# Performance work log

Hardware: AMD Instinct MI355X
Metric: run time of the kernel (lower is better)

## Reference

```python
import jax, jax.numpy as jnp
import numpy as np

N, D = 32768, 256  # n_nodes, in_dim == mem_dim


def setup_inputs() -> dict:
    key = jax.random.key(0)
    ks = jax.random.split(key, 8)
    inputs = jax.random.normal(ks[0], (N, D), jnp.float32)
    state = jax.random.normal(ks[1], (1, D), jnp.float32)  # initial root cell state
    s = 1.0 / np.sqrt(D)  # pytorch default uniform init bound
    root_W = jax.random.uniform(ks[2], (D, D), jnp.float32, -s, s)
    root_b = jax.random.uniform(ks[3], (D,), jnp.float32, -s, s)
    W_ih = jax.random.uniform(ks[4], (4 * D, D), jnp.float32, -s, s)
    W_hh = jax.random.uniform(ks[5], (4 * D, D), jnp.float32, -s, s)
    b_ih = jax.random.uniform(ks[6], (4 * D,), jnp.float32, -s, s)
    b_hh = jax.random.uniform(ks[7], (4 * D,), jnp.float32, -s, s)
    # topologically ordered random tree: parents[i] < i, node 0 is root
    rng = np.random.default_rng(0)
    raw = rng.integers(0, N, size=N)
    parents = jnp.asarray(np.minimum(raw, np.maximum(np.arange(N) - 1, 0)).astype(np.int64))
    idx = jnp.arange(N, dtype=jnp.int64)  # node -> input row (tree.idx)
    return dict(inputs=inputs, state=state, root_W=root_W, root_b=root_b,
                W_ih=W_ih, W_hh=W_hh, b_ih=b_ih, b_hh=b_hh,
                parents=parents, idx=idx)


def reference(inputs, state, root_W, root_b, W_ih, W_hh, b_ih, b_hh, parents, idx):
    n, d = inputs.shape
    # root: tanh(Linear(inputs[root_idx])), cell state = given state
    h0 = jnp.tanh(inputs[idx[0]] @ root_W.T + root_b)
    c0 = state[0]
    H = jnp.zeros((n, d), inputs.dtype).at[0].set(h0)
    C = jnp.zeros((n, d), inputs.dtype).at[0].set(c0)

    def step(carry, i):
        H, C = carry
        p = parents[i]
        x = inputs[idx[i]]
        # torch nn.LSTMCell: gates = x W_ih^T + b_ih + h W_hh^T + b_hh
        gates = x @ W_ih.T + b_ih + H[p] @ W_hh.T + b_hh
        ig, fg, gg, og = jnp.split(gates, 4)
        c = jax.nn.sigmoid(fg) * C[p] + jax.nn.sigmoid(ig) * jnp.tanh(gg)
        h = jax.nn.sigmoid(og) * jnp.tanh(c)
        return (H.at[i].set(h), C.at[i].set(c)), None

    (H, C), _ = jax.lax.scan(step, (H, C), jnp.arange(1, n))
    # topdown_hidden_traversal: scatter each node's hidden into a [n_inputs, mem_dim] buffer
    hiddens = jnp.zeros((n, d), inputs.dtype).at[idx].set(H)
    # (root topdown_state, root topdown hidden, all hiddens)
    return C[0:1], H[0:1], hiddens
```

## Files before the change

### kernel.cpp

```cpp
#include <hip/hip_runtime.h>


#define NN 32768
#define DD 256
#define GP 1024
#define OFFCAP 4096
#define SENT_C 0x7FC00001u
#define SENT_H 0xFFFFFFFFu

typedef __attribute__((ext_vector_type(8))) short short8;
typedef __attribute__((ext_vector_type(4))) float float4_;
typedef __attribute__((ext_vector_type(4))) unsigned uint4_;

static __device__ __forceinline__ unsigned short f2bf(float f) {
    unsigned u = __builtin_bit_cast(unsigned, f);
    unsigned r = u + 0x7FFFu + ((u >> 16) & 1u);
    return (unsigned short)(r >> 16);
}
static __device__ __forceinline__ float bf2f(unsigned short u) {
    unsigned v = ((unsigned)u) << 16;
    return __builtin_bit_cast(float, v);
}
static __device__ __forceinline__ float sigf(float x) { return 1.0f / (1.0f + __expf(-x)); }
static __device__ __forceinline__ float tanh_(float x) { return 1.0f - 2.0f / (__expf(2.0f * x) + 1.0f); }

__global__ void k_init(int* cnt, int* cur, int* maxd, float* C, unsigned* HbU) {
    const int g = blockIdx.x * 256 + threadIdx.x;
    if (g < NN + 2) { cnt[g] = 0; cur[g] = 0; }
    if (g == 0) maxd[0] = 0;
    const uint4_ sc = (uint4_){SENT_C, SENT_C, SENT_C, SENT_C};
    const uint4_ sh = (uint4_){SENT_H, SENT_H, SENT_H, SENT_H};
    uint4_* Cu = (uint4_*)C;
    uint4_* Hu = (uint4_*)HbU;
    #pragma unroll
    for (int k = 0; k < 4; ++k) Cu[(size_t)g + (size_t)k * 524288] = sc;
    #pragma unroll
    for (int k = 0; k < 2; ++k) Hu[(size_t)g + (size_t)k * 524288] = sh;
}

__global__ void k_root(const float* __restrict__ X, const float* __restrict__ state,
                       const float* __restrict__ rootW, const float* __restrict__ rootb,
                       const int* __restrict__ idx,
                       unsigned short* __restrict__ Hb, float* __restrict__ C) {
    const int t = threadIdx.x;
    const int row = idx[0];
    const float4_* xr = (const float4_*)(X + (size_t)row * DD);
    const float4_* wr = (const float4_*)(rootW + (size_t)t * DD);
    float acc = rootb[t];
    for (int k = 0; k < DD / 4; ++k) {
        float4_ a = xr[k], b = wr[k];
        acc += a[0] * b[0] + a[1] * b[1] + a[2] * b[2] + a[3] * b[3];
    }
    Hb[t] = f2bf(tanh_(acc));
    C[t] = state[t];
}

__global__ void k_dep_init(const int* __restrict__ parents, int* dep, int* jmp) {
    int i = blockIdx.x * 256 + threadIdx.x;
    if (i >= NN) return;
    dep[i] = (i == 0) ? 0 : 1;
    jmp[i] = (i == 0) ? 0 : parents[i];
}

__global__ void k_dep_step(const int* __restrict__ depA, const int* __restrict__ jmpA,
                           int* __restrict__ depB, int* __restrict__ jmpB) {
    int i = blockIdx.x * 256 + threadIdx.x;
    if (i >= NN) return;
    int j = jmpA[i];
    depB[i] = depA[i] + depA[j];
    jmpB[i] = jmpA[j];
}

__global__ void k_hist(const int* __restrict__ dep, int* cnt, int* maxd) {
    int i = blockIdx.x * 256 + threadIdx.x;
    if (i >= NN) return;
    int d = dep[i];
    atomicAdd(&cnt[d], 1);
    atomicMax(&maxd[0], d);
}

__global__ void k_scan(const int* __restrict__ cnt, int* __restrict__ off) {
    __shared__ int sums[256];
    const int tid = threadIdx.x;
    const int base = tid * 128;
    int s = 0;
    for (int k = 0; k < 128; ++k) s += cnt[base + k];
    sums[tid] = s;
    __syncthreads();
    if (tid == 0) {
        int run = 0;
        for (int t = 0; t < 256; ++t) { int tmp = sums[t]; sums[t] = run; run += tmp; }
    }
    __syncthreads();
    int run = sums[tid];
    for (int k = 0; k < 128; ++k) { off[base + k] = run; run += cnt[base + k]; }
    if (tid == 255) off[NN] = run;
}

__global__ void k_scatter(const int* __restrict__ dep, const int* __restrict__ off,
                          int* cur, int* __restrict__ lev) {
    int i = blockIdx.x * 256 + threadIdx.x;
    if (i >= NN) return;
    int d = dep[i];
    int pos = off[d] + atomicAdd(&cur[d], 1);
    lev[pos] = i;
}

__global__ __launch_bounds__(256, 1) void k_gx(
    const float* __restrict__ X, const float* __restrict__ Wih,
    const float* __restrict__ bih, const float* __restrict__ bhh,
    const int* __restrict__ idx, unsigned short* __restrict__ Gp) {
    __shared__ __align__(16) short bw_s[128 * 264];
    __shared__ float bias_s[128];
    const int tid = threadIdx.x;
    const int w = tid >> 6, l = tid & 63;
    const int lanelo = l & 15, quad = l >> 4;

    short8 a[2][8];
    #pragma unroll
    for (int ti = 0; ti < 2; ++ti) {
        int n = (blockIdx.x * 8 + w * 2 + ti) * 16 + lanelo;
        int row = idx[n];
        const float* xp = X + (size_t)row * DD + quad * 8;
        #pragma unroll
        for (int ks = 0; ks < 8; ++ks) {
            float4_ x0 = *(const float4_*)(xp + ks * 32);
            float4_ x1 = *(const float4_*)(xp + ks * 32 + 4);
            short8 s;
            s[0] = f2bf(x0[0]); s[1] = f2bf(x0[1]); s[2] = f2bf(x0[2]); s[3] = f2bf(x0[3]);
            s[4] = f2bf(x1[0]); s[5] = f2bf(x1[1]); s[6] = f2bf(x1[2]); s[7] = f2bf(x1[3]);
            a[ti][ks] = s;
        }
    }
    for (int gc = 0; gc < 8; ++gc) {
        __syncthreads();
        for (int e = tid; e < 128 * 64; e += 256) {
            int r = e >> 6, c4 = (e & 63) * 4;
            float4_ b = *(const float4_*)(Wih + (size_t)(gc * 128 + r) * DD + c4);
            unsigned short* pb = (unsigned short*)&bw_s[r * 264 + c4];
            pb[0] = f2bf(b[0]); pb[1] = f2bf(b[1]); pb[2] = f2bf(b[2]); pb[3] = f2bf(b[3]);
        }
        if (tid < 128) bias_s[tid] = bih[gc * 128 + tid] + bhh[gc * 128 + tid];
        __syncthreads();
        #pragma unroll
        for (int ntl = 0; ntl < 8; ++ntl) {
            float4_ acc0 = (float4_){0.f, 0.f, 0.f, 0.f};
            float4_ acc1 = (float4_){0.f, 0.f, 0.f, 0.f};
            #pragma unroll
            for (int ks = 0; ks < 8; ++ks) {
                short8 bf = *(const short8*)&bw_s[(ntl * 16 + lanelo) * 264 + ks * 32 + quad * 8];
                acc0 = __builtin_amdgcn_mfma_f32_16x16x32_bf16(a[0][ks], bf, acc0, 0, 0, 0);
                acc1 = __builtin_amdgcn_mfma_f32_16x16x32_bf16(a[1][ks], bf, acc1, 0, 0, 0);
            }
            float bia = bias_s[ntl * 16 + lanelo];
            int g = gc * 128 + ntl * 16 + lanelo;
            int nb0 = (blockIdx.x * 8 + w * 2) * 16 + quad * 4;
            #pragma unroll
            for (int r = 0; r < 4; ++r) {
                Gp[(size_t)(nb0 + r) * GP + g] = f2bf(acc0[r] + bia);
                Gp[(size_t)(nb0 + 16 + r) * GP + g] = f2bf(acc1[r] + bia);
            }
        }
    }
}

__global__ __launch_bounds__(256, 1) void k_tree2(
    const float* __restrict__ Whh,
    const int* __restrict__ parents,
    const int* __restrict__ off, const int* __restrict__ lev, const int* __restrict__ maxd_g,
    const unsigned short* __restrict__ Gp,
    unsigned short* __restrict__ Hb, float* __restrict__ C) {

    __shared__ __align__(16) short w_s[128 * 264];
    __shared__ __align__(16) short A_s[16 * 264];
    __shared__ __align__(16) float G_s[16 * 128];
    __shared__ __align__(16) float R_s[16 * 132];
    __shared__ int off_s[OFFCAP];
    __shared__ int nd_s[16], par_s[16];

    const int tid = threadIdx.x;
    const int j = blockIdx.x & 7, grp = blockIdx.x >> 3;
    const int w = tid >> 6, l = tid & 63;
    const int lanelo = l & 15, quad = l >> 4;

    for (int e = tid; e < 128 * 64; e += 256) {
        int r = e >> 6, c4 = (e & 63) * 4;
        int G = ((r >> 5) * 256) + j * 32 + (r & 31);
        float4_ b = *(const float4_*)(Whh + (size_t)G * DD + c4);
        unsigned short* pb = (unsigned short*)&w_s[r * 264 + c4];
        pb[0] = f2bf(b[0]); pb[1] = f2bf(b[1]); pb[2] = f2bf(b[2]); pb[3] = f2bf(b[3]);
    }
    const int maxd = maxd_g[0];
    const int staged = (maxd + 2 < OFFCAP) ? (maxd + 2) : OFFCAP;
    for (int e = tid; e < staged; e += 256) off_s[e] = off[e];
    __syncthreads();

    #define OFFS(i) (((i) < staged) ? off_s[(i)] : off[(i)])

    const unsigned* HbU = (const unsigned*)Hb;
    int pn_node = -1, pn_par = 0;
    bool pn_valid = false;

    int lo = OFFS(1);
    for (int d = 1; d <= maxd; ++d) {
        const int hi = OFFS(d + 1);
        const int tiles = (hi - lo + 15) >> 4;
        for (int t = grp; t < tiles; t += 32) {
            const int base = lo + t * 16;
            if (tid < 16) {
                if (pn_valid) {
                    nd_s[tid] = pn_node; par_s[tid] = pn_par;
                } else {
                    int node = -1, p = 0;
                    if (base + tid < hi) { node = lev[base + tid]; p = parents[node]; }
                    nd_s[tid] = node; par_s[tid] = p;
                }
            }
            pn_valid = false;
            __syncthreads();
            {
                int m = tid >> 4, q8 = (tid & 15) * 8;
                int seg = q8 >> 5, cc = q8 & 31;
                float4_ g01 = (float4_){0.f, 0.f, 0.f, 0.f};
                float4_ g23 = (float4_){0.f, 0.f, 0.f, 0.f};
                if (nd_s[m] >= 0) {
                    const unsigned short* gp =
                        Gp + (size_t)nd_s[m] * GP + seg * 256 + j * 32 + cc;
                    short8 gv = *(const short8*)gp;
                    g01[0] = bf2f(gv[0]); g01[1] = bf2f(gv[1]); g01[2] = bf2f(gv[2]); g01[3] = bf2f(gv[3]);
                    g23[0] = bf2f(gv[4]); g23[1] = bf2f(gv[5]); g23[2] = bf2f(gv[6]); g23[3] = bf2f(gv[7]);
                }
                *(float4_*)&G_s[m * 128 + q8] = g01;
                *(float4_*)&G_s[m * 128 + q8 + 4] = g23;
            }
            {
                int nt_base = -1, nt_hi = hi;
                if (t + 32 < tiles) {
                    nt_base = lo + (t + 32) * 16;
                } else if (d < maxd) {
                    const int hi2 = OFFS(d + 2);
                    const int tiles2 = (hi2 - hi + 15) >> 4;
                    if (grp < tiles2) { nt_base = hi + grp * 16; nt_hi = hi2; }
                }
                if (nt_base >= 0) {
                    if (tid < 16) {
                        int node = -1, p = 0;
                        if (nt_base + tid < nt_hi) { node = lev[nt_base + tid]; p = parents[node]; }
                        pn_node = node; pn_par = p;
                    }
                    pn_valid = true;
                }
            }
            const int m0 = tid >> 5, c0 = tid & 31, col = j * 32 + c0;
            float* cpp0 = &C[(size_t)par_s[m0] * DD + col];
            float* cpp1 = &C[(size_t)par_s[m0 + 8] * DD + col];
            float cp0 = __hip_atomic_load(cpp0, __ATOMIC_RELAXED, __HIP_MEMORY_SCOPE_AGENT);
            float cp1 = __hip_atomic_load(cpp1, __ATOMIC_RELAXED, __HIP_MEMORY_SCOPE_AGENT);
            unsigned hv[8];
            bool ok = true;
            #pragma unroll
            for (int k2 = 0; k2 < 8; ++k2) {
                const int e = tid + k2 * 256, m = e >> 7, cu = e & 127;
                hv[k2] = (nd_s[m] >= 0)
                    ? __hip_atomic_load(&HbU[(size_t)par_s[m] * 128 + cu],
                                        __ATOMIC_RELAXED, __HIP_MEMORY_SCOPE_AGENT)
                    : 0u;
                if (nd_s[m] >= 0 && hv[k2] == SENT_H) ok = false;
            }
            if (nd_s[m0] >= 0 && __builtin_bit_cast(unsigned, cp0) == SENT_C) ok = false;
            if (nd_s[m0 + 8] >= 0 && __builtin_bit_cast(unsigned, cp1) == SENT_C) ok = false;
            if (!__syncthreads_and(ok ? 1 : 0)) {
                if (tid < 64) {
                    const int m = tid & 15;
                    const bool act = (tid < 16) && (nd_s[m] >= 0);
                    const unsigned* sp = &HbU[(size_t)par_s[m] * 128 + j * 16];
                    bool miss = act && (__hip_atomic_load(sp, __ATOMIC_RELAXED,
                                                          __HIP_MEMORY_SCOPE_AGENT) == SENT_H);
                    while (__any(miss ? 1 : 0))
                        miss = act && (__hip_atomic_load(sp, __ATOMIC_RELAXED,
                                                         __HIP_MEMORY_SCOPE_AGENT) == SENT_H);
                }
                __syncthreads();
                if (nd_s[m0] >= 0)
                    while (__builtin_bit_cast(unsigned, cp0) == SENT_C) {
                        __builtin_amdgcn_s_sleep(1);
                        cp0 = __hip_atomic_load(cpp0, __ATOMIC_RELAXED, __HIP_MEMORY_SCOPE_AGENT);
                    }
                if (nd_s[m0 + 8] >= 0)
                    while (__builtin_bit_cast(unsigned, cp1) == SENT_C) {
                        __builtin_amdgcn_s_sleep(1);
                        cp1 = __hip_atomic_load(cpp1, __ATOMIC_RELAXED, __HIP_MEMORY_SCOPE_AGENT);
                    }
                #pragma unroll
                for (int k2 = 0; k2 < 8; ++k2) {
                    const int e = tid + k2 * 256, m = e >> 7, cu = e & 127;
                    if (nd_s[m] >= 0)
                        while (hv[k2] == SENT_H) {
                            __builtin_amdgcn_s_sleep(1);
                            hv[k2] = __hip_atomic_load(&HbU[(size_t)par_s[m] * 128 + cu],
                                                       __ATOMIC_RELAXED, __HIP_MEMORY_SCOPE_AGENT);
                        }
                }
            }
            #pragma unroll
            for (int k2 = 0; k2 < 8; ++k2) {
                const int e = tid + k2 * 256, m = e >> 7, cu = e & 127;
                *(unsigned*)&A_s[m * 264 + cu * 2] = hv[k2];
            }
            __syncthreads();
            {
                short8 af[8];
                #pragma unroll
                for (int ks = 0; ks < 8; ++ks)
                    af[ks] = *(const short8*)&A_s[lanelo * 264 + ks * 32 + quad * 8];
                #pragma unroll
                for (int ti = 0; ti < 2; ++ti) {
                    int ntl = w * 2 + ti;
                    float4_ acc = (float4_){0.f, 0.f, 0.f, 0.f};
                    #pragma unroll
                    for (int ks = 0; ks < 8; ++ks) {
                        short8 bf = *(const short8*)&w_s[(ntl * 16 + lanelo) * 264 + ks * 32 + quad * 8];
                        acc = __builtin_amdgcn_mfma_f32_16x16x32_bf16(af[ks], bf, acc, 0, 0, 0);
                    }
                    #pragma unroll
                    for (int r = 0; r < 4; ++r)
                        R_s[(quad * 4 + r) * 132 + ntl * 16 + lanelo] = acc[r];
                }
            }
            __syncthreads();
            {
                #pragma unroll
                for (int pass = 0; pass < 2; ++pass) {
                    int m = m0 + pass * 8;
                    float cp = pass ? cp1 : cp0;
                    float ig = R_s[m * 132 + c0]      + G_s[m * 128 + c0];
                    float fg = R_s[m * 132 + 32 + c0] + G_s[m * 128 + 32 + c0];
                    float gg = R_s[m * 132 + 64 + c0] + G_s[m * 128 + 64 + c0];
                    float og = R_s[m * 132 + 96 + c0] + G_s[m * 128 + 96 + c0];
                    float cn = sigf(fg) * cp + sigf(ig) * tanh_(gg);
                    float hn = sigf(og) * tanh_(cn);
                    int node = nd_s[m];
                    unsigned short hs = f2bf(hn);
                    unsigned pair = ((unsigned)hs) |
                                    (((unsigned)(unsigned short)__shfl_down((int)hs, 1)) << 16);
                    if (node >= 0) {
                        __hip_atomic_store(&C[(size_t)node * DD + col], cn,
                                           __ATOMIC_RELAXED, __HIP_MEMORY_SCOPE_AGENT);
                        if ((c0 & 1) == 0)
                            __hip_atomic_store(&((unsigned*)Hb)[(size_t)node * 128 + (col >> 1)],
                                               pair, __ATOMIC_RELAXED, __HIP_MEMORY_SCOPE_AGENT);
                    }
                }
            }
            __builtin_amdgcn_fence(__ATOMIC_RELEASE, "workgroup");
            __syncthreads();
        }
        lo = hi;
    }
    #undef OFFS
}

__global__ void k_out(const unsigned short* __restrict__ Hb, const float* __restrict__ C,
                      const int* __restrict__ idx, float* __restrict__ out) {
    const int b = blockIdx.x, t = threadIdx.x;
    if (b < NN) {
        int drow = idx[b];
        out[512 + (size_t)drow * DD + t] = bf2f(Hb[(size_t)b * DD + t]);
    } else {
        out[t] = C[t];
        out[DD + t] = bf2f(Hb[t]);
    }
}

extern "C" void kernel_launch(void* const* d_in, const int* in_sizes, int n_in,
                              void* d_out, int out_size, void* d_ws, size_t ws_size,
                              hipStream_t stream) {
    const float* X     = (const float*)d_in[0];
    const float* state = (const float*)d_in[1];
    const float* rootW = (const float*)d_in[2];
    const float* rootb = (const float*)d_in[3];
    const float* Wih   = (const float*)d_in[4];
    const float* Whh   = (const float*)d_in[5];
    const float* bih   = (const float*)d_in[6];
    const float* bhh   = (const float*)d_in[7];
    const int* parents = (const int*)d_in[8];
    const int* idx     = (const int*)d_in[9];

    float* C           = (float*)d_ws;
    unsigned short* Hb = (unsigned short*)(C + (size_t)NN * DD);
    unsigned short* Gp = Hb + (size_t)NN * DD;
    int* ip            = (int*)(Gp + (size_t)NN * GP);
    int* depA = ip;            ip += NN;
    int* jmpA = ip;            ip += NN;
    int* depB = ip;            ip += NN;
    int* jmpB = ip;            ip += NN;
    int* cnt  = ip;            ip += NN + 2;
    int* off  = ip;            ip += NN + 2;
    int* cur  = ip;            ip += NN + 2;
    int* lev  = ip;            ip += NN;
    int* maxd = ip;            ip += 4;
    float* out = (float*)d_out;

    k_init<<<dim3(2048), dim3(256), 0, stream>>>(cnt, cur, maxd, C, (unsigned*)Hb);
    k_root<<<dim3(1), dim3(256), 0, stream>>>(X, state, rootW, rootb, idx, Hb, C);

    k_dep_init<<<dim3(128), dim3(256), 0, stream>>>(parents, depA, jmpA);
    int* dA = depA; int* jA = jmpA; int* dB = depB; int* jB = jmpB;
    for (int it = 0; it < 15; ++it) {
        k_dep_step<<<dim3(128), dim3(256), 0, stream>>>(dA, jA, dB, jB);
        int* tp;
        tp = dA; dA = dB; dB = tp;
        tp = jA; jA = jB; jB = tp;
    }
    k_hist<<<dim3(128), dim3(256), 0, stream>>>(dA, cnt, maxd);
    k_scan<<<dim3(1), dim3(256), 0, stream>>>(cnt, off);
    k_scatter<<<dim3(128), dim3(256), 0, stream>>>(dA, off, cur, lev);

    k_gx<<<dim3(256), dim3(256), 0, stream>>>(X, Wih, bih, bhh, idx, Gp);
    k_tree2<<<dim3(256), dim3(256), 0, stream>>>(Whh, parents, off, lev, maxd, Gp, Hb, C);
    k_out<<<dim3(NN + 1), dim3(256), 0, stream>>>(Hb, C, idx, out);
}
```

Baseline: 1.764 ms.

## Fuse LSTM gate epilogue into MFMA registers by permuting W_hh rows

Reorders the W_hh rows staged in shared memory so each wave's two MFMA accumulators hold matching i/g and f/o gate columns. The gate nonlinearities are then computed directly from registers using lane shuffles, which removes the R_s shared-memory round trip and one __syncthreads per tile. Parent cell-state loads now follow the MFMA output layout, so only half the lanes do them. The init kernel is also split, and the sentinel poisoning plus root kernel are moved to run right before the tree kernel.

```diff
diff --git a/kernel.cpp b/kernel.cpp
--- a/kernel.cpp
+++ b/kernel.cpp
@@ -12,6 +12,9 @@
 typedef __attribute__((ext_vector_type(4))) float float4_;
 typedef __attribute__((ext_vector_type(4))) unsigned uint4_;
 
+#define ATL(p) __hip_atomic_load((p), __ATOMIC_RELAXED, __HIP_MEMORY_SCOPE_AGENT)
+#define ATS(p, v) __hip_atomic_store((p), (v), __ATOMIC_RELAXED, __HIP_MEMORY_SCOPE_AGENT)
+
 static __device__ __forceinline__ unsigned short f2bf(float f) {
     unsigned u = __builtin_bit_cast(unsigned, f);
     unsigned r = u + 0x7FFFu + ((u >> 16) & 1u);
@@ -24,10 +27,14 @@
 static __device__ __forceinline__ float sigf(float x) { return 1.0f / (1.0f + __expf(-x)); }
 static __device__ __forceinline__ float tanh_(float x) { return 1.0f - 2.0f / (__expf(2.0f * x) + 1.0f); }
 
-__global__ void k_init(int* cnt, int* cur, int* maxd, float* C, unsigned* HbU) {
-    const int g = blockIdx.x * 256 + threadIdx.x;
+__global__ void k_init_sched(int* cnt, int* cur, int* maxd) {
+    int g = blockIdx.x * 256 + threadIdx.x;
     if (g < NN + 2) { cnt[g] = 0; cur[g] = 0; }
     if (g == 0) maxd[0] = 0;
+}
+
+__global__ void k_poison(float* C, unsigned* HbU) {
+    const int g = blockIdx.x * 256 + threadIdx.x;
     const uint4_ sc = (uint4_){SENT_C, SENT_C, SENT_C, SENT_C};
     const uint4_ sh = (uint4_){SENT_H, SENT_H, SENT_H, SENT_H};
     uint4_* Cu = (uint4_*)C;
@@ -174,7 +181,6 @@
     __shared__ __align__(16) short w_s[128 * 264];
     __shared__ __align__(16) short A_s[16 * 264];
     __shared__ __align__(16) float G_s[16 * 128];
-    __shared__ __align__(16) float R_s[16 * 132];
     __shared__ int off_s[OFFCAP];
     __shared__ int nd_s[16], par_s[16];
 
@@ -182,10 +188,16 @@
     const int j = blockIdx.x & 7, grp = blockIdx.x >> 3;
     const int w = tid >> 6, l = tid & 63;
     const int lanelo = l & 15, quad = l >> 4;
+    const bool ewl = (lanelo < 8);
+    const int colw = j * 32 + w * 8 + (lanelo & 7);
+    const int gcw = w * 8 + (lanelo & 7);
+    const int gof0 = (lanelo >> 3) * 32 + gcw;
+    const int gof1 = gof0 + 64;
 
     for (int e = tid; e < 128 * 64; e += 256) {
         int r = e >> 6, c4 = (e & 63) * 4;
-        int G = ((r >> 5) * 256) + j * 32 + (r & 31);
+        int wp = r >> 5, ti = (r >> 4) & 1, n = r & 15;
+        int G = (ti * 2 + (n >> 3)) * 256 + j * 32 + wp * 8 + (n & 7);
         float4_ b = *(const float4_*)(Whh + (size_t)G * DD + c4);
         unsigned short* pb = (unsigned short*)&w_s[r * 264 + c4];
         pb[0] = f2bf(b[0]); pb[1] = f2bf(b[1]); pb[2] = f2bf(b[2]); pb[3] = f2bf(b[3]);
@@ -198,6 +210,8 @@
     #define OFFS(i) (((i) < staged) ? off_s[(i)] : off[(i)])
 
     const unsigned* HbU = (const unsigned*)Hb;
+    unsigned* HbW = (unsigned*)Hb;
+    const unsigned* Cw = (const unsigned*)C;
     int pn_node = -1, pn_par = 0;
     bool pn_valid = false;
 
@@ -251,54 +265,49 @@
                     pn_valid = true;
                 }
             }
-            const int m0 = tid >> 5, c0 = tid & 31, col = j * 32 + c0;
-            float* cpp0 = &C[(size_t)par_s[m0] * DD + col];
-            float* cpp1 = &C[(size_t)par_s[m0 + 8] * DD + col];
-            float cp0 = __hip_atomic_load(cpp0, __ATOMIC_RELAXED, __HIP_MEMORY_SCOPE_AGENT);
-            float cp1 = __hip_atomic_load(cpp1, __ATOMIC_RELAXED, __HIP_MEMORY_SCOPE_AGENT);
             unsigned hv[8];
             bool ok = true;
             #pragma unroll
             for (int k2 = 0; k2 < 8; ++k2) {
                 const int e = tid + k2 * 256, m = e >> 7, cu = e & 127;
                 hv[k2] = (nd_s[m] >= 0)
-                    ? __hip_atomic_load(&HbU[(size_t)par_s[m] * 128 + cu],
-                                        __ATOMIC_RELAXED, __HIP_MEMORY_SCOPE_AGENT)
-                    : 0u;
+                    ? ATL(&HbU[(size_t)par_s[m] * 128 + cu]) : 0u;
                 if (nd_s[m] >= 0 && hv[k2] == SENT_H) ok = false;
             }
-            if (nd_s[m0] >= 0 && __builtin_bit_cast(unsigned, cp0) == SENT_C) ok = false;
-            if (nd_s[m0 + 8] >= 0 && __builtin_bit_cast(unsigned, cp1) == SENT_C) ok = false;
+            unsigned cwv[4];
+            #pragma unroll
+            for (int r = 0; r < 4; ++r) {
+                const int m = quad * 4 + r;
+                cwv[r] = (ewl && nd_s[m] >= 0)
+                    ? ATL(&Cw[(size_t)par_s[m] * DD + colw]) : 0u;
+                if (ewl && nd_s[m] >= 0 && cwv[r] == SENT_C) ok = false;
+            }
             if (!__syncthreads_and(ok ? 1 : 0)) {
                 if (tid < 64) {
                     const int m = tid & 15;
                     const bool act = (tid < 16) && (nd_s[m] >= 0);
                     const unsigned* sp = &HbU[(size_t)par_s[m] * 128 + j * 16];
-                    bool miss = act && (__hip_atomic_load(sp, __ATOMIC_RELAXED,
-                                                          __HIP_MEMORY_SCOPE_AGENT) == SENT_H);
+                    bool miss = act && (ATL(sp) == SENT_H);
                     while (__any(miss ? 1 : 0))
-                        miss = act && (__hip_atomic_load(sp, __ATOMIC_RELAXED,
-                                                         __HIP_MEMORY_SCOPE_AGENT) == SENT_H);
+                        miss = act && (ATL(sp) == SENT_H);
                 }
                 __syncthreads();
-                if (nd_s[m0] >= 0)
-                    while (__builtin_bit_cast(unsigned, cp0) == SENT_C) {
-                        __builtin_amdgcn_s_sleep(1);
-                        cp0 = __hip_atomic_load(cpp0, __ATOMIC_RELAXED, __HIP_MEMORY_SCOPE_AGENT);
-                    }
-                if (nd_s[m0 + 8] >= 0)
-                    while (__builtin_bit_cast(unsigned, cp1) == SENT_C) {
-                        __builtin_amdgcn_s_sleep(1);
-                        cp1 = __hip_atomic_load(cpp1, __ATOMIC_RELAXED, __HIP_MEMORY_SCOPE_AGENT);
-                    }
                 #pragma unroll
                 for (int k2 = 0; k2 < 8; ++k2) {
                     const int e = tid + k2 * 256, m = e >> 7, cu = e & 127;
                     if (nd_s[m] >= 0)
                         while (hv[k2] == SENT_H) {
                             __builtin_amdgcn_s_sleep(1);
-                            hv[k2] = __hip_atomic_load(&HbU[(size_t)par_s[m] * 128 + cu],
-                                                       __ATOMIC_RELAXED, __HIP_MEMORY_SCOPE_AGENT);
+                            hv[k2] = ATL(&HbU[(size_t)par_s[m] * 128 + cu]);
+                        }
+                }
+                #pragma unroll
+                for (int r = 0; r < 4; ++r) {
+                    const int m = quad * 4 + r;
+                    if (ewl && nd_s[m] >= 0)
+                        while (cwv[r] == SENT_C) {
+                            __builtin_amdgcn_s_sleep(1);
+                            cwv[r] = ATL(&Cw[(size_t)par_s[m] * DD + colw]);
                         }
                 }
             }
@@ -308,48 +317,38 @@
                 *(unsigned*)&A_s[m * 264 + cu * 2] = hv[k2];
             }
             __syncthreads();
+            float4_ acc0 = (float4_){0.f, 0.f, 0.f, 0.f};
+            float4_ acc1 = (float4_){0.f, 0.f, 0.f, 0.f};
             {
                 short8 af[8];
                 #pragma unroll
                 for (int ks = 0; ks < 8; ++ks)
                     af[ks] = *(const short8*)&A_s[lanelo * 264 + ks * 32 + quad * 8];
                 #pragma unroll
-                for (int ti = 0; ti < 2; ++ti) {
-                    int ntl = w * 2 + ti;
-                    float4_ acc = (float4_){0.f, 0.f, 0.f, 0.f};
-                    #pragma unroll
-                    for (int ks = 0; ks < 8; ++ks) {
-                        short8 bf = *(const short8*)&w_s[(ntl * 16 + lanelo) * 264 + ks * 32 + quad * 8];
-                        acc = __builtin_amdgcn_mfma_f32_16x16x32_bf16(af[ks], bf, acc, 0, 0, 0);
-                    }
-                    #pragma unroll
-                    for (int r = 0; r < 4; ++r)
-                        R_s[(quad * 4 + r) * 132 + ntl * 16 + lanelo] = acc[r];
-                }
-            }
-            __syncthreads();
-            {
-                #pragma unroll
-                for (int pass = 0; pass < 2; ++pass) {
-                    int m = m0 + pass * 8;
-                    float cp = pass ? cp1 : cp0;
-                    float ig = R_s[m * 132 + c0]      + G_s[m * 128 + c0];
-                    float fg = R_s[m * 132 + 32 + c0] + G_s[m * 128 + 32 + c0];
-                    float gg = R_s[m * 132 + 64 + c0] + G_s[m * 128 + 64 + c0];
-                    float og = R_s[m * 132 + 96 + c0] + G_s[m * 128 + 96 + c0];
-                    float cn = sigf(fg) * cp + sigf(ig) * tanh_(gg);
-                    float hn = sigf(og) * tanh_(cn);
-                    int node = nd_s[m];
-                    unsigned short hs = f2bf(hn);
-                    unsigned pair = ((unsigned)hs) |
-                                    (((unsigned)(unsigned short)__shfl_down((int)hs, 1)) << 16);
-                    if (node >= 0) {
-                        __hip_atomic_store(&C[(size_t)node * DD + col], cn,
-                                           __ATOMIC_RELAXED, __HIP_MEMORY_SCOPE_AGENT);
-                        if ((c0 & 1) == 0)
-                            __hip_atomic_store(&((unsigned*)Hb)[(size_t)node * 128 + (col >> 1)],
-                                               pair, __ATOMIC_RELAXED, __HIP_MEMORY_SCOPE_AGENT);
-                    }
+                for (int ks = 0; ks < 8; ++ks) {
+                    short8 b0 = *(const short8*)&w_s[(w * 32 + lanelo) * 264 + ks * 32 + quad * 8];
+                    short8 b1 = *(const short8*)&w_s[(w * 32 + 16 + lanelo) * 264 + ks * 32 + quad * 8];
+                    acc0 = __builtin_amdgcn_mfma_f32_16x16x32_bf16(af[ks], b0, acc0, 0, 0, 0);
+                    acc1 = __builtin_amdgcn_mfma_f32_16x16x32_bf16(af[ks], b1, acc1, 0, 0, 0);
+                }
+            }
+            #pragma unroll
+            for (int r = 0; r < 4; ++r) {
+                const int m = quad * 4 + r;
+                float a0 = acc0[r] + G_s[m * 128 + gof0];
+                float a1 = acc1[r] + G_s[m * 128 + gof1];
+                float fg = __shfl_xor(a0, 8);
+                float og = __shfl_xor(a1, 8);
+                float cp = __builtin_bit_cast(float, cwv[r]);
+                float cn = sigf(fg) * cp + sigf(a0) * tanh_(a1);
+                float hn = sigf(og) * tanh_(cn);
+                unsigned short hs = f2bf(hn);
+                unsigned pair = ((unsigned)hs) |
+                                (((unsigned)(unsigned short)__shfl_down((int)hs, 1)) << 16);
+                if (ewl && nd_s[m] >= 0) {
+                    ATS(&C[(size_t)nd_s[m] * DD + colw], cn);
+                    if ((lanelo & 1) == 0)
+                        ATS(&HbW[(size_t)nd_s[m] * 128 + (colw >> 1)], pair);
                 }
             }
             __builtin_amdgcn_fence(__ATOMIC_RELEASE, "workgroup");
@@ -398,12 +397,10 @@
     int* off  = ip;            ip += NN + 2;
     int* cur  = ip;            ip += NN + 2;
     int* lev  = ip;            ip += NN;
-    int* maxd = ip;            ip += 4;
+    int* maxd = ip;            ip += 8;
     float* out = (float*)d_out;
 
-    k_init<<<dim3(2048), dim3(256), 0, stream>>>(cnt, cur, maxd, C, (unsigned*)Hb);
-    k_root<<<dim3(1), dim3(256), 0, stream>>>(X, state, rootW, rootb, idx, Hb, C);
-
+    k_init_sched<<<dim3(129), dim3(256), 0, stream>>>(cnt, cur, maxd);
     k_dep_init<<<dim3(128), dim3(256), 0, stream>>>(parents, depA, jmpA);
     int* dA = depA; int* jA = jmpA; int* dB = depB; int* jB = jmpB;
     for (int it = 0; it < 15; ++it) {
@@ -417,6 +414,9 @@
     k_scatter<<<dim3(128), dim3(256), 0, stream>>>(dA, off, cur, lev);
 
     k_gx<<<dim3(256), dim3(256), 0, stream>>>(X, Wih, bih, bhh, idx, Gp);
+
+    k_poison<<<dim3(2048), dim3(256), 0, stream>>>(C, (unsigned*)Hb);
+    k_root<<<dim3(1), dim3(256), 0, stream>>>(X, state, rootW, rootb, idx, Hb, C);
     k_tree2<<<dim3(256), dim3(256), 0, stream>>>(Whh, parents, off, lev, maxd, Gp, Hb, C);
     k_out<<<dim3(NN + 1), dim3(256), 0, stream>>>(Hb, C, idx, out);
 }
```

Result: slower. 2.446 ms (+38.7%).
